# Performance work log

Hardware: AMD Instinct MI355X
Metric: run time of the kernel (lower is better)

Reference implementation:

```python
import jax, jax.numpy as jnp
import numpy as np

N_NODES = 100000
N_EDGES = 1600000
IN_FEATS = 128
HIDDEN = 64
LAYERS = 3
LN_EPS = 1e-5


def setup_inputs() -> dict:
    key = jax.random.key(0)
    ks = jax.random.split(key, 5)
    inputs = jax.random.normal(ks[0], (N_NODES, IN_FEATS), dtype=jnp.float32)
    src = jax.random.randint(ks[1], (N_EDGES,), 0, N_NODES, dtype=jnp.int32)
    dst = jax.random.randint(ks[2], (N_EDGES,), 0, N_NODES, dtype=jnp.int32)
    Ws = jax.random.normal(ks[3], (LAYERS, IN_FEATS, HIDDEN), dtype=jnp.float32) * 0.05
    bs = jax.random.normal(ks[4], (LAYERS, HIDDEN), dtype=jnp.float32) * 0.05
    gammas = jnp.ones((LAYERS, HIDDEN), dtype=jnp.float32)
    betas = jnp.zeros((LAYERS, HIDDEN), dtype=jnp.float32)
    return {"inputs": inputs, "src": src, "dst": dst, "Ws": Ws, "bs": bs,
            "gammas": gammas, "betas": betas}


def _mlp(x, W, b, gamma, beta):
    # Linear -> LayerNorm -> ReLU (torch defaults, eps=1e-5)
    h = x @ W + b
    mu = jnp.mean(h, axis=-1, keepdims=True)
    var = jnp.mean(jnp.square(h - mu), axis=-1, keepdims=True)
    h = (h - mu) * jax.lax.rsqrt(var + LN_EPS) * gamma + beta
    return jax.nn.relu(h)


def _gcn(h, src, dst, deg_mask):
    # copy_src message + per-destination max reduce; nodes with no
    # incoming edges keep their own feature (DGL recv semantics).
    msg = h[src]                                           # [E, HIDDEN]
    agg = jax.ops.segment_max(msg, dst, num_segments=N_NODES)
    agg = jnp.where(deg_mask, agg, h)
    return jnp.concatenate([h, agg], axis=1)               # [N, 2*HIDDEN]


def reference(inputs, src, dst, Ws, bs, gammas, betas):
    deg = jax.ops.segment_sum(jnp.ones((dst.shape[0],), jnp.float32), dst,
                              num_segments=N_NODES)
    deg_mask = (deg > 0)[:, None]
    v = inputs
    for i in range(LAYERS):
        v = _mlp(v, Ws[i], bs[i], gammas[i], betas[i])
        v = _gcn(v, src, dst, deg_mask)
    return v
```

## Files before the change

### kernel.cpp

```cpp
#include <hip/hip_runtime.h>

#define NN 100000
#define NE 1600000
#define INF 128
#define HID 64
#define LN_EPS 1e-5f

#define BINB 9
#define BINSZ 512
#define NBIN 196
#define FILLB 512
#define BCAP 9250

typedef unsigned short u16;
typedef __attribute__((ext_vector_type(8))) short bf16x8;
typedef __attribute__((ext_vector_type(4))) float f32x4;

#define SAP 136

__device__ __forceinline__ u16 f2bf(float f) {
    unsigned u = __float_as_uint(f);
    return (u16)((u + 0x7FFFu + ((u >> 16) & 1u)) >> 16);
}
__device__ __forceinline__ unsigned pack2bf(float a, float b) {
    unsigned ua = __float_as_uint(a), ub = __float_as_uint(b);
    ua = (ua + 0x7FFFu + ((ua >> 16) & 1u)) >> 16;
    ub = (ub + 0x7FFFu + ((ub >> 16) & 1u)) >> 16;
    return ua | (ub << 16);
}


__global__ __launch_bounds__(256) void k_zero(int* __restrict__ bincur) {
    int i = threadIdx.x;
    if (i < NBIN) bincur[i] = 0;
}

__global__ __launch_bounds__(256) void k_binfill(const int* __restrict__ src, const int* __restrict__ dst,
                                                 int* __restrict__ bincur, unsigned* __restrict__ binpair) {
    __shared__ int cnt[NBIN];
    __shared__ int base[NBIN];
    __shared__ int cur[NBIN];
    int tid = threadIdx.x;
    const int chunk = (NE + FILLB - 1) / FILLB;
    int s = blockIdx.x * chunk;
    int t = min(s + chunk, NE);

    for (int i = tid; i < NBIN; i += 256) cnt[i] = 0;
    __syncthreads();
    for (int e = s + tid; e < t; e += 256) atomicAdd(&cnt[dst[e] >> BINB], 1);
    __syncthreads();
    for (int i = tid; i < NBIN; i += 256) {
        int c = cnt[i];
        base[i] = c ? atomicAdd(&bincur[i], c) : 0;
        cur[i] = 0;
    }
    __syncthreads();
    for (int e = s + tid; e < t; e += 256) {
        int d = dst[e];
        int b = d >> BINB;
        int pos = base[b] + atomicAdd(&cur[b], 1);
        binpair[(size_t)b * BCAP + pos] = ((unsigned)src[e] << BINB) | (unsigned)(d & (BINSZ - 1));
    }
}

__global__ __launch_bounds__(256) void k_binsort(const unsigned* __restrict__ binpair,
                                                 const int* __restrict__ bincur,
                                                 int* __restrict__ rowptr, int* __restrict__ deg,
                                                 int* __restrict__ eidx) {
    __shared__ int cnt[BINSZ];
    __shared__ int ofs[BINSZ];
    __shared__ int cur[BINSZ];
    int tid = threadIdx.x, lane = tid & 63, wid = tid >> 6;
    int b = blockIdx.x;
    int s = b * BCAP;
    int t = s + bincur[b];

    cnt[tid] = 0; cnt[tid + 256] = 0;
    __syncthreads();
    for (int e = s + tid; e < t; e += 256) atomicAdd(&cnt[binpair[e] & (BINSZ - 1)], 1);
    __syncthreads();

    int a0 = cnt[2 * tid], a1 = cnt[2 * tid + 1];
    int ps = a0 + a1;
    int v = ps;
    #pragma unroll
    for (int d = 1; d < 64; d <<= 1) { int y = __shfl_up(v, d); if (lane >= d) v += y; }
    __shared__ int wsum[4];
    if (lane == 63) wsum[wid] = v;
    __syncthreads();
    int add = 0;
    for (int w = 0; w < wid; ++w) add += wsum[w];
    int excl = v + add - ps;
    ofs[2 * tid] = excl; ofs[2 * tid + 1] = excl + a0;
    cur[2 * tid] = excl; cur[2 * tid + 1] = excl + a0;
    __syncthreads();

    int nodeBase = b << BINB;
    #pragma unroll
    for (int j = 0; j < 2; ++j) {
        int i = tid + j * 256;
        int n = nodeBase + i;
        if (n < NN) { rowptr[n] = s + ofs[i]; deg[n] = cnt[i]; }
    }

    for (int e = s + tid; e < t; e += 256) {
        unsigned p = binpair[e];
        int l = p & (BINSZ - 1);
        int pos = s + atomicAdd(&cur[l], 1);
        eidx[pos] = (int)(p >> BINB);
    }
}


__global__ __launch_bounds__(256) void k_wconv(const float* __restrict__ Ws, u16* __restrict__ wtb) {
    int L = blockIdx.x, tid = threadIdx.x;
    int c = tid & 63, k0 = (tid >> 6) * 32;
    const float* W = Ws + (size_t)L * INF * HID;
    alignas(16) u16 tmp[32];
    #pragma unroll
    for (int k = 0; k < 32; ++k) tmp[k] = f2bf(W[(size_t)(k0 + k) * HID + c]);
    u16* dstp = wtb + (size_t)L * HID * INF + (size_t)c * INF + k0;
    #pragma unroll
    for (int j = 0; j < 4; ++j)
        *(uint4*)(dstp + j * 8) = *(uint4*)&tmp[j * 8];
}


template<int KIND>
__global__ __launch_bounds__(256) void k_mlp(
    const float* __restrict__ fin,
    u16* xbf,
    const u16* __restrict__ wtb,
    const float* __restrict__ bias, const float* __restrict__ gam, const float* __restrict__ bet,
    float* __restrict__ fout)
{
    __shared__ u16 sA[64 * SAP];
    __shared__ u16 sB[64 * SAP];

    const int tid = threadIdx.x, lane = tid & 63;
    const int w = __builtin_amdgcn_readfirstlane(tid >> 6);
    const int node0 = blockIdx.x * 64;

    if (KIND == 0) {
        #pragma unroll
        for (int j = 0; j < 8; ++j) {
            int f4 = tid + j * 256;
            int nl = f4 >> 5, k4 = f4 & 31;
            int n = node0 + nl; if (n >= NN) n = NN - 1;
            float4 v = *(const float4*)(fin + (size_t)n * INF + k4 * 4);
            *(uint2*)&sA[nl * SAP + k4 * 4] = make_uint2(pack2bf(v.x, v.y), pack2bf(v.z, v.w));
        }
    } else {
        #pragma unroll
        for (int j = 0; j < 4; ++j) {
            int ch = tid + j * 256;
            int nl = ch >> 4, c8 = ch & 15;
            int n = node0 + nl; if (n >= NN) n = NN - 1;
            *(uint4*)&sA[nl * SAP + c8 * 8] = *(const uint4*)(xbf + (size_t)n * INF + c8 * 8);
        }
    }
    #pragma unroll
    for (int j = 0; j < 4; ++j) {
        int ch = tid + j * 256;
        int r = ch >> 4, k8 = ch & 15;
        *(uint4*)&sB[r * SAP + k8 * 8] = *(const uint4*)(wtb + (size_t)r * INF + k8 * 8);
    }

    const int cl = lane & 15;
    float bC[4], gC[4], tC[4];
    #pragma unroll
    for (int nt = 0; nt < 4; ++nt) {
        int c = nt * 16 + cl;
        bC[nt] = bias[c]; gC[nt] = gam[c]; tC[nt] = bet[c];
    }

    __syncthreads();

    f32x4 acc[4] = {(f32x4)0.f, (f32x4)0.f, (f32x4)0.f, (f32x4)0.f};
    const int kg = (lane >> 4) * 8;
    #pragma unroll
    for (int kk = 0; kk < 4; ++kk) {
        bf16x8 a = *(const bf16x8*)&sA[(w * 16 + cl) * SAP + kk * 32 + kg];
        #pragma unroll
        for (int nt = 0; nt < 4; ++nt) {
            bf16x8 b = *(const bf16x8*)&sB[(nt * 16 + cl) * SAP + kk * 32 + kg];
            acc[nt] = __builtin_amdgcn_mfma_f32_16x16x32_bf16(a, b, acc[nt], 0, 0, 0);
        }
    }

    #pragma unroll
    for (int nt = 0; nt < 4; ++nt)
        #pragma unroll
        for (int r = 0; r < 4; ++r) acc[nt][r] += bC[nt];

    float mu[4], rs[4];
    #pragma unroll
    for (int r = 0; r < 4; ++r) {
        float s = acc[0][r] + acc[1][r] + acc[2][r] + acc[3][r];
        float q = acc[0][r]*acc[0][r] + acc[1][r]*acc[1][r] + acc[2][r]*acc[2][r] + acc[3][r]*acc[3][r];
        #pragma unroll
        for (int m = 1; m < 16; m <<= 1) { s += __shfl_xor(s, m); q += __shfl_xor(q, m); }
        mu[r] = s * 0.015625f;
        float var = fmaxf(q * 0.015625f - mu[r] * mu[r], 0.f);
        rs[r] = rsqrtf(var + LN_EPS);
    }

    #pragma unroll
    for (int nt = 0; nt < 4; ++nt) {
        int c = nt * 16 + cl;
        #pragma unroll
        for (int r = 0; r < 4; ++r) {
            int row = w * 16 + (lane >> 4) * 4 + r;
            float o = fmaxf((acc[nt][r] - mu[r]) * rs[r] * gC[nt] + tC[nt], 0.f);
            sA[row * SAP + c] = f2bf(o);
            if (KIND == 2) {
                int n = node0 + row;
                if (n < NN) fout[(size_t)n * 128 + c] = o;
            }
        }
    }

    #pragma unroll
    for (int i = 0; i < 2; ++i) {
        int ch = lane + i * 64;
        int r16 = ch >> 3, c8 = ch & 7;
        int row = w * 16 + r16;
        int n = node0 + row;
        if (n < NN)
            *(uint4*)(xbf + (size_t)n * INF + c8 * 8) = *(const uint4*)&sA[row * SAP + c8 * 8];
    }
}


#define GMAX4(v) { m0 = max(m0, v.x & 0xFFFFu); m1 = max(m1, v.x >> 16); \
                   m2 = max(m2, v.y & 0xFFFFu); m3 = max(m3, v.y >> 16); }

__global__ __launch_bounds__(256) void k_gather_bb(
    const u16* __restrict__ hb, const int* __restrict__ rowptr, const int* __restrict__ deg,
    const int* __restrict__ eidx, u16* __restrict__ aggb)
{
    int tid = threadIdx.x, lane = tid & 63, wid = tid >> 6;
    int nw0 = blockIdx.x * 16 + wid * 4;
    int g = lane >> 4, fl = lane & 15;
    int n = nw0 + g;

    int rp = (lane < 4) ? rowptr[nw0 + lane] : 0;
    int dv = (lane < 4) ? deg[nw0 + lane] : 0;
    int start = __shfl(rp, g);
    int dg    = __shfl(dv, g);

    unsigned m0 = 0, m1 = 0, m2 = 0, m3 = 0;
    if (dg == 0) {
        uint2 v = *(const uint2*)(hb + (size_t)n * 128 + fl * 4);
        m0 = v.x & 0xFFFFu; m1 = v.x >> 16; m2 = v.y & 0xFFFFu; m3 = v.y >> 16;
    } else {
        int e = start, endv = start + dg;
        for (; e + 8 <= endv; e += 8) {
            int i0 = eidx[e],     i1 = eidx[e + 1], i2 = eidx[e + 2], i3 = eidx[e + 3];
            int i4 = eidx[e + 4], i5 = eidx[e + 5], i6 = eidx[e + 6], i7 = eidx[e + 7];
            uint2 v0 = *(const uint2*)(hb + (size_t)i0 * 128 + fl * 4);
            uint2 v1 = *(const uint2*)(hb + (size_t)i1 * 128 + fl * 4);
            uint2 v2 = *(const uint2*)(hb + (size_t)i2 * 128 + fl * 4);
            uint2 v3 = *(const uint2*)(hb + (size_t)i3 * 128 + fl * 4);
            uint2 v4 = *(const uint2*)(hb + (size_t)i4 * 128 + fl * 4);
            uint2 v5 = *(const uint2*)(hb + (size_t)i5 * 128 + fl * 4);
            uint2 v6 = *(const uint2*)(hb + (size_t)i6 * 128 + fl * 4);
            uint2 v7 = *(const uint2*)(hb + (size_t)i7 * 128 + fl * 4);
            GMAX4(v0); GMAX4(v1); GMAX4(v2); GMAX4(v3);
            GMAX4(v4); GMAX4(v5); GMAX4(v6); GMAX4(v7);
        }
        for (; e < endv; ++e) {
            uint2 v = *(const uint2*)(hb + (size_t)eidx[e] * 128 + fl * 4);
            GMAX4(v);
        }
    }
    uint2 o; o.x = m0 | (m1 << 16); o.y = m2 | (m3 << 16);
    *(uint2*)(aggb + (size_t)n * 128 + fl * 4) = o;
}

__global__ __launch_bounds__(256) void k_gather_bf(
    const u16* __restrict__ hb, const int* __restrict__ rowptr, const int* __restrict__ deg,
    const int* __restrict__ eidx, float* __restrict__ out)
{
    int tid = threadIdx.x, lane = tid & 63, wid = tid >> 6;
    int nw0 = blockIdx.x * 16 + wid * 4;
    int g = lane >> 4, fl = lane & 15;
    int n = nw0 + g;

    int rp = (lane < 4) ? rowptr[nw0 + lane] : 0;
    int dv = (lane < 4) ? deg[nw0 + lane] : 0;
    int start = __shfl(rp, g);
    int dg    = __shfl(dv, g);

    if (dg == 0) {
        float4 v = *(const float4*)(out + (size_t)n * 128 + fl * 4);
        *(float4*)(out + (size_t)n * 128 + 64 + fl * 4) = v;
        return;
    }

    unsigned m0 = 0, m1 = 0, m2 = 0, m3 = 0;
    int e = start, endv = start + dg;
    for (; e + 8 <= endv; e += 8) {
        int i0 = eidx[e],     i1 = eidx[e + 1], i2 = eidx[e + 2], i3 = eidx[e + 3];
        int i4 = eidx[e + 4], i5 = eidx[e + 5], i6 = eidx[e + 6], i7 = eidx[e + 7];
        uint2 v0 = *(const uint2*)(hb + (size_t)i0 * 128 + fl * 4);
        uint2 v1 = *(const uint2*)(hb + (size_t)i1 * 128 + fl * 4);
        uint2 v2 = *(const uint2*)(hb + (size_t)i2 * 128 + fl * 4);
        uint2 v3 = *(const uint2*)(hb + (size_t)i3 * 128 + fl * 4);
        uint2 v4 = *(const uint2*)(hb + (size_t)i4 * 128 + fl * 4);
        uint2 v5 = *(const uint2*)(hb + (size_t)i5 * 128 + fl * 4);
        uint2 v6 = *(const uint2*)(hb + (size_t)i6 * 128 + fl * 4);
        uint2 v7 = *(const uint2*)(hb + (size_t)i7 * 128 + fl * 4);
        GMAX4(v0); GMAX4(v1); GMAX4(v2); GMAX4(v3);
        GMAX4(v4); GMAX4(v5); GMAX4(v6); GMAX4(v7);
    }
    for (; e < endv; ++e) {
        uint2 v = *(const uint2*)(hb + (size_t)eidx[e] * 128 + fl * 4);
        GMAX4(v);
    }
    float4 o = make_float4(__uint_as_float(m0 << 16), __uint_as_float(m1 << 16),
                           __uint_as_float(m2 << 16), __uint_as_float(m3 << 16));
    *(float4*)(out + (size_t)n * 128 + 64 + fl * 4) = o;
}


extern "C" void kernel_launch(void* const* d_in, const int* in_sizes, int n_in,
                              void* d_out, int out_size, void* d_ws, size_t ws_size,
                              hipStream_t stream) {
    const float* inputs = (const float*)d_in[0];
    const int*   src    = (const int*)d_in[1];
    const int*   dst    = (const int*)d_in[2];
    const float* Ws     = (const float*)d_in[3];
    const float* bs     = (const float*)d_in[4];
    const float* gs     = (const float*)d_in[5];
    const float* bes    = (const float*)d_in[6];
    float* out = (float*)d_out;

    char* w = (char*)d_ws;
    int* bincur = (int*)w; w += 256 * 4;
    int* rowptr = (int*)w; w += (size_t)(NN + 1) * 4;
    int* deg    = (int*)w; w += (size_t)NN * 4;
    int* eidx   = (int*)w; w += (size_t)NBIN * BCAP * 4;
    uintptr_t a = (uintptr_t)w; a = (a + 255) & ~(uintptr_t)255; w = (char*)a;
    u16* wtb     = (u16*)w; w += 3 * (size_t)INF * HID * 2;
    u16* xbf     = (u16*)w; w += (size_t)NN * INF * 2;
    unsigned* binpair = (unsigned*)w; w += (size_t)NBIN * BCAP * 4;

    const int MLPB = (NN + 63) / 64;
    const int GATB = (NN + 15) / 16;

    k_zero   <<<1,     256, 0, stream>>>(bincur);
    k_binfill<<<FILLB, 256, 0, stream>>>(src, dst, bincur, binpair);
    k_binsort<<<NBIN,  256, 0, stream>>>(binpair, bincur, rowptr, deg, eidx);

    k_wconv<<<3, 256, 0, stream>>>(Ws, wtb);

    k_mlp<0><<<MLPB, 256, 0, stream>>>(inputs, xbf, wtb,            bs,       gs,       bes,       nullptr);
    k_gather_bb<<<GATB, 256, 0, stream>>>(xbf, rowptr, deg, eidx, xbf + 64);
    k_mlp<1><<<MLPB, 256, 0, stream>>>(nullptr, xbf, wtb + 8192,    bs + 64,  gs + 64,  bes + 64,  nullptr);
    k_gather_bb<<<GATB, 256, 0, stream>>>(xbf, rowptr, deg, eidx, xbf + 64);
    k_mlp<2><<<MLPB, 256, 0, stream>>>(nullptr, xbf, wtb + 16384,   bs + 128, gs + 128, bes + 128, out);
    k_gather_bf<<<GATB, 256, 0, stream>>>(xbf, rowptr, deg, eidx, out);
}
```

Before: 190.1 us.

## Slice hidden features into 4 planar arrays so gather reads a compact table

The MLP kernel now writes its 64-wide bf16 output twice: once row-major as xh, and once split into four 16-feature slices stored as separate planar arrays. The gather kernels launch one block group per slice, each handling 16 nodes per wave with 4 lanes per node, so each pass randomly gathers from a 3.2 MB table instead of a strided 25.6 MB buffer. The intent is to improve L2/MALL hit rates on random gathers. Edge indices are also loaded and results stored with nontemporal hints. In exchange, each edge list is read four times, the MLP writes extra data, and the gathers use narrower 8-byte accesses.

```diff
diff --git a/kernel.cpp b/kernel.cpp
--- a/kernel.cpp
+++ b/kernel.cpp
@@ -11,10 +11,12 @@
 #define NBIN 196
 #define FILLB 512
 #define BCAP 9250
+#define NN16 ((size_t)NN * 16)
 
 typedef unsigned short u16;
 typedef __attribute__((ext_vector_type(8))) short bf16x8;
 typedef __attribute__((ext_vector_type(4))) float f32x4;
+typedef __attribute__((ext_vector_type(2))) unsigned u32x2;
 
 #define SAP 136
 
@@ -129,7 +131,8 @@
 template<int KIND>
 __global__ __launch_bounds__(256) void k_mlp(
     const float* __restrict__ fin,
-    u16* xbf,
+    u16* xh, const u16* __restrict__ xa,
+    u16* __restrict__ ht,
     const u16* __restrict__ wtb,
     const float* __restrict__ bias, const float* __restrict__ gam, const float* __restrict__ bet,
     float* __restrict__ fout)
@@ -156,7 +159,9 @@
             int ch = tid + j * 256;
             int nl = ch >> 4, c8 = ch & 15;
             int n = node0 + nl; if (n >= NN) n = NN - 1;
-            *(uint4*)&sA[nl * SAP + c8 * 8] = *(const uint4*)(xbf + (size_t)n * INF + c8 * 8);
+            const u16* p = (c8 < 8) ? (xh + (size_t)n * HID + c8 * 8)
+                                    : (xa + (size_t)n * HID + (c8 - 8) * 8);
+            *(uint4*)&sA[nl * SAP + c8 * 8] = *(const uint4*)p;
         }
     }
     #pragma unroll
@@ -222,12 +227,25 @@
 
     #pragma unroll
     for (int i = 0; i < 2; ++i) {
-        int ch = lane + i * 64;
-        int r16 = ch >> 3, c8 = ch & 7;
+        int ch = i * 64 + lane;
+        int r16 = ch & 15, q = ch >> 4;
+        int sl = q >> 1, half = q & 1;
         int row = w * 16 + r16;
         int n = node0 + row;
         if (n < NN)
-            *(uint4*)(xbf + (size_t)n * INF + c8 * 8) = *(const uint4*)&sA[row * SAP + c8 * 8];
+            *(uint4*)(ht + (size_t)sl * NN16 + (size_t)n * 16 + half * 8) =
+                *(const uint4*)&sA[row * SAP + sl * 16 + half * 8];
+    }
+    if (KIND != 2) {
+        #pragma unroll
+        for (int i = 0; i < 2; ++i) {
+            int ch = i * 64 + lane;
+            int r16 = ch >> 3, c8 = ch & 7;
+            int row = w * 16 + r16;
+            int n = node0 + row;
+            if (n < NN)
+                *(uint4*)(xh + (size_t)n * HID + c8 * 8) = *(const uint4*)&sA[row * SAP + c8 * 8];
+        }
     }
 }
 
@@ -236,91 +254,114 @@
                    m2 = max(m2, v.y & 0xFFFFu); m3 = max(m3, v.y >> 16); }
 
 __global__ __launch_bounds__(256) void k_gather_bb(
-    const u16* __restrict__ hb, const int* __restrict__ rowptr, const int* __restrict__ deg,
-    const int* __restrict__ eidx, u16* __restrict__ aggb)
+    const u16* __restrict__ ht, const int* __restrict__ rowptr, const int* __restrict__ deg,
+    const int* __restrict__ eidx, u16* __restrict__ xa)
 {
     int tid = threadIdx.x, lane = tid & 63, wid = tid >> 6;
-    int nw0 = blockIdx.x * 16 + wid * 4;
-    int g = lane >> 4, fl = lane & 15;
+    int sl = blockIdx.x & 3;
+    int nb = blockIdx.x >> 2;
+    int nw0 = nb * 64 + wid * 16;
+    int g = lane >> 2, fl = lane & 3;
     int n = nw0 + g;
-
-    int rp = (lane < 4) ? rowptr[nw0 + lane] : 0;
-    int dv = (lane < 4) ? deg[nw0 + lane] : 0;
+    if (n >= NN) return;
+
+    int rp = (lane < 16) ? rowptr[min(nw0 + lane, NN - 1)] : 0;
+    int dv = (lane < 16) ? deg[min(nw0 + lane, NN - 1)] : 0;
     int start = __shfl(rp, g);
     int dg    = __shfl(dv, g);
 
+    const u16* hp = ht + (size_t)sl * NN16 + fl * 4;
     unsigned m0 = 0, m1 = 0, m2 = 0, m3 = 0;
     if (dg == 0) {
-        uint2 v = *(const uint2*)(hb + (size_t)n * 128 + fl * 4);
+        uint2 v = *(const uint2*)(hp + (size_t)n * 16);
         m0 = v.x & 0xFFFFu; m1 = v.x >> 16; m2 = v.y & 0xFFFFu; m3 = v.y >> 16;
     } else {
         int e = start, endv = start + dg;
         for (; e + 8 <= endv; e += 8) {
-            int i0 = eidx[e],     i1 = eidx[e + 1], i2 = eidx[e + 2], i3 = eidx[e + 3];
-            int i4 = eidx[e + 4], i5 = eidx[e + 5], i6 = eidx[e + 6], i7 = eidx[e + 7];
-            uint2 v0 = *(const uint2*)(hb + (size_t)i0 * 128 + fl * 4);
-            uint2 v1 = *(const uint2*)(hb + (size_t)i1 * 128 + fl * 4);
-            uint2 v2 = *(const uint2*)(hb + (size_t)i2 * 128 + fl * 4);
-            uint2 v3 = *(const uint2*)(hb + (size_t)i3 * 128 + fl * 4);
-            uint2 v4 = *(const uint2*)(hb + (size_t)i4 * 128 + fl * 4);
-            uint2 v5 = *(const uint2*)(hb + (size_t)i5 * 128 + fl * 4);
-            uint2 v6 = *(const uint2*)(hb + (size_t)i6 * 128 + fl * 4);
-            uint2 v7 = *(const uint2*)(hb + (size_t)i7 * 128 + fl * 4);
+            int i0 = __builtin_nontemporal_load(eidx + e);
+            int i1 = __builtin_nontemporal_load(eidx + e + 1);
+            int i2 = __builtin_nontemporal_load(eidx + e + 2);
+            int i3 = __builtin_nontemporal_load(eidx + e + 3);
+            int i4 = __builtin_nontemporal_load(eidx + e + 4);
+            int i5 = __builtin_nontemporal_load(eidx + e + 5);
+            int i6 = __builtin_nontemporal_load(eidx + e + 6);
+            int i7 = __builtin_nontemporal_load(eidx + e + 7);
+            uint2 v0 = *(const uint2*)(hp + (size_t)i0 * 16);
+            uint2 v1 = *(const uint2*)(hp + (size_t)i1 * 16);
+            uint2 v2 = *(const uint2*)(hp + (size_t)i2 * 16);
+            uint2 v3 = *(const uint2*)(hp + (size_t)i3 * 16);
+            uint2 v4 = *(const uint2*)(hp + (size_t)i4 * 16);
+            uint2 v5 = *(const uint2*)(hp + (size_t)i5 * 16);
+            uint2 v6 = *(const uint2*)(hp + (size_t)i6 * 16);
+            uint2 v7 = *(const uint2*)(hp + (size_t)i7 * 16);
             GMAX4(v0); GMAX4(v1); GMAX4(v2); GMAX4(v3);
             GMAX4(v4); GMAX4(v5); GMAX4(v6); GMAX4(v7);
         }
         for (; e < endv; ++e) {
-            uint2 v = *(const uint2*)(hb + (size_t)eidx[e] * 128 + fl * 4);
+            int i = __builtin_nontemporal_load(eidx + e);
+            uint2 v = *(const uint2*)(hp + (size_t)i * 16);
             GMAX4(v);
         }
     }
-    uint2 o; o.x = m0 | (m1 << 16); o.y = m2 | (m3 << 16);
-    *(uint2*)(aggb + (size_t)n * 128 + fl * 4) = o;
+    u32x2 o; o.x = m0 | (m1 << 16); o.y = m2 | (m3 << 16);
+    __builtin_nontemporal_store(o, (u32x2*)(xa + (size_t)n * HID + sl * 16 + fl * 4));
 }
 
 __global__ __launch_bounds__(256) void k_gather_bf(
-    const u16* __restrict__ hb, const int* __restrict__ rowptr, const int* __restrict__ deg,
+    const u16* __restrict__ ht, const int* __restrict__ rowptr, const int* __restrict__ deg,
     const int* __restrict__ eidx, float* __restrict__ out)
 {
     int tid = threadIdx.x, lane = tid & 63, wid = tid >> 6;
-    int nw0 = blockIdx.x * 16 + wid * 4;
-    int g = lane >> 4, fl = lane & 15;
+    int sl = blockIdx.x & 3;
+    int nb = blockIdx.x >> 2;
+    int nw0 = nb * 64 + wid * 16;
+    int g = lane >> 2, fl = lane & 3;
     int n = nw0 + g;
-
-    int rp = (lane < 4) ? rowptr[nw0 + lane] : 0;
-    int dv = (lane < 4) ? deg[nw0 + lane] : 0;
+    if (n >= NN) return;
+
+    int rp = (lane < 16) ? rowptr[min(nw0 + lane, NN - 1)] : 0;
+    int dv = (lane < 16) ? deg[min(nw0 + lane, NN - 1)] : 0;
     int start = __shfl(rp, g);
     int dg    = __shfl(dv, g);
 
     if (dg == 0) {
-        float4 v = *(const float4*)(out + (size_t)n * 128 + fl * 4);
-        *(float4*)(out + (size_t)n * 128 + 64 + fl * 4) = v;
+        f32x4 v = *(const f32x4*)(out + (size_t)n * 128 + sl * 16 + fl * 4);
+        __builtin_nontemporal_store(v, (f32x4*)(out + (size_t)n * 128 + 64 + sl * 16 + fl * 4));
         return;
     }
 
+    const u16* hp = ht + (size_t)sl * NN16 + fl * 4;
     unsigned m0 = 0, m1 = 0, m2 = 0, m3 = 0;
     int e = start, endv = start + dg;
     for (; e + 8 <= endv; e += 8) {
-        int i0 = eidx[e],     i1 = eidx[e + 1], i2 = eidx[e + 2], i3 = eidx[e + 3];
-        int i4 = eidx[e + 4], i5 = eidx[e + 5], i6 = eidx[e + 6], i7 = eidx[e + 7];
-        uint2 v0 = *(const uint2*)(hb + (size_t)i0 * 128 + fl * 4);
-        uint2 v1 = *(const uint2*)(hb + (size_t)i1 * 128 + fl * 4);
-        uint2 v2 = *(const uint2*)(hb + (size_t)i2 * 128 + fl * 4);
-        uint2 v3 = *(const uint2*)(hb + (size_t)i3 * 128 + fl * 4);
-        uint2 v4 = *(const uint2*)(hb + (size_t)i4 * 128 + fl * 4);
-        uint2 v5 = *(const uint2*)(hb + (size_t)i5 * 128 + fl * 4);
-        uint2 v6 = *(const uint2*)(hb + (size_t)i6 * 128 + fl * 4);
-        uint2 v7 = *(const uint2*)(hb + (size_t)i7 * 128 + fl * 4);
+        int i0 = __builtin_nontemporal_load(eidx + e);
+        int i1 = __builtin_nontemporal_load(eidx + e + 1);
+        int i2 = __builtin_nontemporal_load(eidx + e + 2);
+        int i3 = __builtin_nontemporal_load(eidx + e + 3);
+        int i4 = __builtin_nontemporal_load(eidx + e + 4);
+        int i5 = __builtin_nontemporal_load(eidx + e + 5);
+        int i6 = __builtin_nontemporal_load(eidx + e + 6);
+        int i7 = __builtin_nontemporal_load(eidx + e + 7);
+        uint2 v0 = *(const uint2*)(hp + (size_t)i0 * 16);
+        uint2 v1 = *(const uint2*)(hp + (size_t)i1 * 16);
+        uint2 v2 = *(const uint2*)(hp + (size_t)i2 * 16);
+        uint2 v3 = *(const uint2*)(hp + (size_t)i3 * 16);
+        uint2 v4 = *(const uint2*)(hp + (size_t)i4 * 16);
+        uint2 v5 = *(const uint2*)(hp + (size_t)i5 * 16);
+        uint2 v6 = *(const uint2*)(hp + (size_t)i6 * 16);
+        uint2 v7 = *(const uint2*)(hp + (size_t)i7 * 16);
         GMAX4(v0); GMAX4(v1); GMAX4(v2); GMAX4(v3);
         GMAX4(v4); GMAX4(v5); GMAX4(v6); GMAX4(v7);
     }
     for (; e < endv; ++e) {
-        uint2 v = *(const uint2*)(hb + (size_t)eidx[e] * 128 + fl * 4);
+        int i = __builtin_nontemporal_load(eidx + e);
+        uint2 v = *(const uint2*)(hp + (size_t)i * 16);
         GMAX4(v);
     }
-    float4 o = make_float4(__uint_as_float(m0 << 16), __uint_as_float(m1 << 16),
-                           __uint_as_float(m2 << 16), __uint_as_float(m3 << 16));
-    *(float4*)(out + (size_t)n * 128 + 64 + fl * 4) = o;
+    f32x4 o;
+    o[0] = __uint_as_float(m0 << 16); o[1] = __uint_as_float(m1 << 16);
+    o[2] = __uint_as_float(m2 << 16); o[3] = __uint_as_float(m3 << 16);
+    __builtin_nontemporal_store(o, (f32x4*)(out + (size_t)n * 128 + 64 + sl * 16 + fl * 4));
 }
 
 
@@ -342,12 +383,14 @@
     int* deg    = (int*)w; w += (size_t)NN * 4;
     int* eidx   = (int*)w; w += (size_t)NBIN * BCAP * 4;
     uintptr_t a = (uintptr_t)w; a = (a + 255) & ~(uintptr_t)255; w = (char*)a;
-    u16* wtb     = (u16*)w; w += 3 * (size_t)INF * HID * 2;
-    u16* xbf     = (u16*)w; w += (size_t)NN * INF * 2;
+    u16* wtb = (u16*)w; w += 3 * (size_t)INF * HID * 2;
+    u16* xh  = (u16*)w; w += (size_t)NN * HID * 2;
+    u16* xa  = (u16*)w; w += (size_t)NN * HID * 2;
+    u16* ht  = (u16*)w; w += 4 * NN16 * 2;
     unsigned* binpair = (unsigned*)w; w += (size_t)NBIN * BCAP * 4;
 
     const int MLPB = (NN + 63) / 64;
-    const int GATB = (NN + 15) / 16;
+    const int GATB = ((NN + 63) / 64) * 4;
 
     k_zero   <<<1,     256, 0, stream>>>(bincur);
     k_binfill<<<FILLB, 256, 0, stream>>>(src, dst, bincur, binpair);
@@ -355,10 +398,13 @@
 
     k_wconv<<<3, 256, 0, stream>>>(Ws, wtb);
 
-    k_mlp<0><<<MLPB, 256, 0, stream>>>(inputs, xbf, wtb,            bs,       gs,       bes,       nullptr);
-    k_gather_bb<<<GATB, 256, 0, stream>>>(xbf, rowptr, deg, eidx, xbf + 64);
-    k_mlp<1><<<MLPB, 256, 0, stream>>>(nullptr, xbf, wtb + 8192,    bs + 64,  gs + 64,  bes + 64,  nullptr);
-    k_gather_bb<<<GATB, 256, 0, stream>>>(xbf, rowptr, deg, eidx, xbf + 64);
-    k_mlp<2><<<MLPB, 256, 0, stream>>>(nullptr, xbf, wtb + 16384,   bs + 128, gs + 128, bes + 128, out);
-    k_gather_bf<<<GATB, 256, 0, stream>>>(xbf, rowptr, deg, eidx, out);
-}
+    k_mlp<0><<<MLPB, 256, 0, stream>>>(inputs, xh, nullptr, ht, wtb,
+                                       bs, gs, bes, nullptr);
+    k_gather_bb<<<GATB, 256, 0, stream>>>(ht, rowptr, deg, eidx, xa);
+    k_mlp<1><<<MLPB, 256, 0, stream>>>(nullptr, xh, xa, ht, wtb + 8192,
+                                       bs + 64, gs + 64, bes + 64, nullptr);
+    k_gather_bb<<<GATB, 256, 0, stream>>>(ht, rowptr, deg, eidx, xa);
+    k_mlp<2><<<MLPB, 256, 0, stream>>>(nullptr, xh, xa, ht, wtb + 16384,
+                                       bs + 128, gs + 128, bes + 128, out);
+    k_gather_bf<<<GATB, 256, 0, stream>>>(ht, rowptr, deg, eidx, out);
+}
```

Result: slower. 326.8 us (+71.9%).

## Sort nodes by in-degree so gather wavefronts process similar-degree nodes

Applied to the files above, without the earlier changes.

Adds a degree histogram, a scan and a counting-sort pass that build a degree-ordered node permutation together with permuted rowptr and degree arrays. The gather kernels then process nodes in that order, so each wavefront's four node groups have similar edge counts and less divergence or idle lanes. The cost is three extra small preprocessing kernels, plus writes to output rows that are no longer contiguous within a wavefront. With random graphs (mean degree 16, Poisson) the imbalance being removed is moderate.

```diff
diff --git a/kernel.cpp b/kernel.cpp
--- a/kernel.cpp
+++ b/kernel.cpp
@@ -11,6 +11,7 @@
 #define NBIN 196
 #define FILLB 512
 #define BCAP 9250
+#define DBK 64
 
 typedef unsigned short u16;
 typedef __attribute__((ext_vector_type(8))) short bf16x8;
@@ -30,9 +31,10 @@
 }
 
 
-__global__ __launch_bounds__(256) void k_zero(int* __restrict__ bincur) {
+__global__ __launch_bounds__(256) void k_zero(int* __restrict__ bincur, int* __restrict__ dtot) {
     int i = threadIdx.x;
     if (i < NBIN) bincur[i] = 0;
+    if (i < DBK) dtot[i] = 0;
 }
 
 __global__ __launch_bounds__(256) void k_binfill(const int* __restrict__ src, const int* __restrict__ dst,
@@ -112,6 +114,56 @@
 }
 
 
+__global__ __launch_bounds__(256) void k_dhist(const int* __restrict__ deg, int* __restrict__ dtot) {
+    __shared__ int h[DBK];
+    int tid = threadIdx.x;
+    if (tid < DBK) h[tid] = 0;
+    __syncthreads();
+    int n = blockIdx.x * 256 + tid;
+    if (n < NN) atomicAdd(&h[min(deg[n], DBK - 1)], 1);
+    __syncthreads();
+    if (tid < DBK && h[tid]) atomicAdd(&dtot[tid], h[tid]);
+}
+
+__global__ __launch_bounds__(64) void k_dscan(const int* __restrict__ dtot, int* __restrict__ dcur) {
+    int lane = threadIdx.x;
+    int x = dtot[lane];
+    int v = x;
+    #pragma unroll
+    for (int d = 1; d < 64; d <<= 1) { int y = __shfl_up(v, d); if (lane >= d) v += y; }
+    int total = __shfl(v, 63);
+    dcur[lane] = total - v;
+}
+
+__global__ __launch_bounds__(256) void k_dfill(const int* __restrict__ deg, const int* __restrict__ rowptr,
+                                               int* __restrict__ dcur, int* __restrict__ perm,
+                                               int* __restrict__ rowptrP, int* __restrict__ degP) {
+    __shared__ int cnt[DBK];
+    __shared__ int base[DBK];
+    __shared__ int cur[DBK];
+    int tid = threadIdx.x;
+    int n = blockIdx.x * 256 + tid;
+    int b = (n < NN) ? min(deg[n], DBK - 1) : -1;
+
+    if (tid < DBK) cnt[tid] = 0;
+    __syncthreads();
+    if (b >= 0) atomicAdd(&cnt[b], 1);
+    __syncthreads();
+    if (tid < DBK) {
+        int c = cnt[tid];
+        base[tid] = c ? atomicAdd(&dcur[tid], c) : 0;
+        cur[tid] = 0;
+    }
+    __syncthreads();
+    if (b >= 0) {
+        int pos = base[b] + atomicAdd(&cur[b], 1);
+        perm[pos] = n;
+        rowptrP[pos] = rowptr[n];
+        degP[pos] = deg[n];
+    }
+}
+
+
 __global__ __launch_bounds__(256) void k_wconv(const float* __restrict__ Ws, u16* __restrict__ wtb) {
     int L = blockIdx.x, tid = threadIdx.x;
     int c = tid & 63, k0 = (tid >> 6) * 32;
@@ -236,16 +288,17 @@
                    m2 = max(m2, v.y & 0xFFFFu); m3 = max(m3, v.y >> 16); }
 
 __global__ __launch_bounds__(256) void k_gather_bb(
-    const u16* __restrict__ hb, const int* __restrict__ rowptr, const int* __restrict__ deg,
+    const u16* __restrict__ hb, const int* __restrict__ perm,
+    const int* __restrict__ rowptrP, const int* __restrict__ degP,
     const int* __restrict__ eidx, u16* __restrict__ aggb)
 {
     int tid = threadIdx.x, lane = tid & 63, wid = tid >> 6;
     int nw0 = blockIdx.x * 16 + wid * 4;
     int g = lane >> 4, fl = lane & 15;
-    int n = nw0 + g;
-
-    int rp = (lane < 4) ? rowptr[nw0 + lane] : 0;
-    int dv = (lane < 4) ? deg[nw0 + lane] : 0;
+
+    int pn = 0, rp = 0, dv = 0;
+    if (lane < 4) { int i = nw0 + lane; pn = perm[i]; rp = rowptrP[i]; dv = degP[i]; }
+    int n     = __shfl(pn, g);
     int start = __shfl(rp, g);
     int dg    = __shfl(dv, g);
 
@@ -279,16 +332,17 @@
 }
 
 __global__ __launch_bounds__(256) void k_gather_bf(
-    const u16* __restrict__ hb, const int* __restrict__ rowptr, const int* __restrict__ deg,
+    const u16* __restrict__ hb, const int* __restrict__ perm,
+    const int* __restrict__ rowptrP, const int* __restrict__ degP,
     const int* __restrict__ eidx, float* __restrict__ out)
 {
     int tid = threadIdx.x, lane = tid & 63, wid = tid >> 6;
     int nw0 = blockIdx.x * 16 + wid * 4;
     int g = lane >> 4, fl = lane & 15;
-    int n = nw0 + g;
-
-    int rp = (lane < 4) ? rowptr[nw0 + lane] : 0;
-    int dv = (lane < 4) ? deg[nw0 + lane] : 0;
+
+    int pn = 0, rp = 0, dv = 0;
+    if (lane < 4) { int i = nw0 + lane; pn = perm[i]; rp = rowptrP[i]; dv = degP[i]; }
+    int n     = __shfl(pn, g);
     int start = __shfl(rp, g);
     int dg    = __shfl(dv, g);
 
@@ -337,28 +391,37 @@
     float* out = (float*)d_out;
 
     char* w = (char*)d_ws;
-    int* bincur = (int*)w; w += 256 * 4;
-    int* rowptr = (int*)w; w += (size_t)(NN + 1) * 4;
-    int* deg    = (int*)w; w += (size_t)NN * 4;
-    int* eidx   = (int*)w; w += (size_t)NBIN * BCAP * 4;
+    int* bincur  = (int*)w; w += 256 * 4;
+    int* dtot    = (int*)w; w += DBK * 4;
+    int* dcur    = (int*)w; w += DBK * 4;
+    int* rowptr  = (int*)w; w += (size_t)(NN + 1) * 4;
+    int* deg     = (int*)w; w += (size_t)NN * 4;
+    int* perm    = (int*)w; w += (size_t)NN * 4;
+    int* rowptrP = (int*)w; w += (size_t)NN * 4;
+    int* degP    = (int*)w; w += (size_t)NN * 4;
+    int* eidx    = (int*)w; w += (size_t)NBIN * BCAP * 4;
     uintptr_t a = (uintptr_t)w; a = (a + 255) & ~(uintptr_t)255; w = (char*)a;
-    u16* wtb     = (u16*)w; w += 3 * (size_t)INF * HID * 2;
-    u16* xbf     = (u16*)w; w += (size_t)NN * INF * 2;
+    u16* wtb = (u16*)w; w += 3 * (size_t)INF * HID * 2;
+    u16* xbf = (u16*)w; w += (size_t)NN * INF * 2;
     unsigned* binpair = (unsigned*)w; w += (size_t)NBIN * BCAP * 4;
 
     const int MLPB = (NN + 63) / 64;
     const int GATB = (NN + 15) / 16;
-
-    k_zero   <<<1,     256, 0, stream>>>(bincur);
+    const int NB   = (NN + 255) / 256;
+
+    k_zero   <<<1,     256, 0, stream>>>(bincur, dtot);
     k_binfill<<<FILLB, 256, 0, stream>>>(src, dst, bincur, binpair);
     k_binsort<<<NBIN,  256, 0, stream>>>(binpair, bincur, rowptr, deg, eidx);
+    k_dhist  <<<NB, 256, 0, stream>>>(deg, dtot);
+    k_dscan  <<<1,   64, 0, stream>>>(dtot, dcur);
+    k_dfill  <<<NB, 256, 0, stream>>>(deg, rowptr, dcur, perm, rowptrP, degP);
 
     k_wconv<<<3, 256, 0, stream>>>(Ws, wtb);
 
-    k_mlp<0><<<MLPB, 256, 0, stream>>>(inputs, xbf, wtb,            bs,       gs,       bes,       nullptr);
-    k_gather_bb<<<GATB, 256, 0, stream>>>(xbf, rowptr, deg, eidx, xbf + 64);
-    k_mlp<1><<<MLPB, 256, 0, stream>>>(nullptr, xbf, wtb + 8192,    bs + 64,  gs + 64,  bes + 64,  nullptr);
-    k_gather_bb<<<GATB, 256, 0, stream>>>(xbf, rowptr, deg, eidx, xbf + 64);
-    k_mlp<2><<<MLPB, 256, 0, stream>>>(nullptr, xbf, wtb + 16384,   bs + 128, gs + 128, bes + 128, out);
-    k_gather_bf<<<GATB, 256, 0, stream>>>(xbf, rowptr, deg, eidx, out);
-}
+    k_mlp<0><<<MLPB, 256, 0, stream>>>(inputs, xbf, wtb,          bs,       gs,       bes,       nullptr);
+    k_gather_bb<<<GATB, 256, 0, stream>>>(xbf, perm, rowptrP, degP, eidx, xbf + 64);
+    k_mlp<1><<<MLPB, 256, 0, stream>>>(nullptr, xbf, wtb + 8192,  bs + 64,  gs + 64,  bes + 64,  nullptr);
+    k_gather_bb<<<GATB, 256, 0, stream>>>(xbf, perm, rowptrP, degP, eidx, xbf + 64);
+    k_mlp<2><<<MLPB, 256, 0, stream>>>(nullptr, xbf, wtb + 16384, bs + 128, gs + 128, bes + 128, out);
+    k_gather_bf<<<GATB, 256, 0, stream>>>(xbf, perm, rowptrP, degP, eidx, out);
+}
```

Result: slower. 200.9 us (+5.6%).
